# Kernel tuning notes

Measured on AMD Instinct MI355X. Metric: run time of the kernel, lower is better.

The kernel has to match this reference:

```python
import jax, jax.numpy as jnp
import numpy as np

H = 1024   # hidden_size
S = 1024   # seq_length
B = 32     # batch_size


def setup_inputs() -> dict:
    key = jax.random.key(0)
    k1, k2, k3, k4, k5, k6 = jax.random.split(key, 6)
    scale = 1.0 / np.sqrt(3 * H)
    return {
        "encoder_states": jax.random.normal(k1, (S, B, 2 * H), dtype=jnp.float32),
        "hidden": jax.random.normal(k2, (B, H), dtype=jnp.float32),
        "cell": jax.random.normal(k3, (B, H), dtype=jnp.float32),
        "W_attn": jax.random.normal(k4, (H, 3 * H), dtype=jnp.float32) * scale,
        "b_attn": jax.random.normal(k5, (H,), dtype=jnp.float32) * scale,
        "v_w": jax.random.normal(k6, (H,), dtype=jnp.float32) * (1.0 / np.sqrt(H)),
    }


def reference(encoder_states, hidden, cell, W_attn, b_attn, v_w):
    # cell is accepted by the original forward but unused.
    # Split the concat-linear into two projections (mathematically identical,
    # avoids materializing the repeated hidden + concat tensor):
    # cat((hidden_rep, enc), -1) @ W.T == hidden @ W[:, :H].T + enc @ W[:, H:].T
    W_h = W_attn[:, :H]          # [H, H]   multiplies decoder hidden
    W_e = W_attn[:, H:]          # [H, 2H]  multiplies encoder states
    enc = jnp.transpose(encoder_states, (1, 0, 2))          # [B, S, 2H]
    h_proj = hidden @ W_h.T + b_attn                         # [B, H], broadcast over S
    e_proj = jnp.einsum("bse,he->bsh", enc, W_e)             # [B, S, H]
    energy = jnp.tanh(h_proj[:, None, :] + e_proj)           # [B, S, H]
    attention = jnp.einsum("bsh,h->bs", energy, v_w)         # [B, S]
    return jax.nn.softmax(attention, axis=1)
```

## Files before the change

### kernel.cpp

```cpp
#include <hip/hip_runtime.h>
#include <hip/hip_bf16.h>

#define H 1024
#define S 1024
#define B 32
#define K2 2048

typedef unsigned short u16;
typedef __attribute__((ext_vector_type(8))) short short8;
typedef __attribute__((ext_vector_type(8))) unsigned short u16x8;
typedef __attribute__((ext_vector_type(4))) float floatx4;

__device__ __forceinline__ u16 f2bf(float f) {
  unsigned u = __float_as_uint(f);
  u += 0x7FFFu + ((u >> 16) & 1u);
  return (u16)(u >> 16);
}

__device__ __forceinline__ void gld_lds16(const void* g, void* l) {
  __builtin_amdgcn_global_load_lds(
      (const __attribute__((address_space(1))) unsigned int*)g,
      (__attribute__((address_space(3))) unsigned int*)l, 16, 0, 0);
}

__device__ __forceinline__ float tanh_fast(float x) {
  float t = __expf(2.0f * x);
  return 1.0f - 2.0f / (t + 1.0f);
}

__global__ void conv_we_k(const float* __restrict__ W, u16* __restrict__ dst) {
  const int h = blockIdx.x;
  const int t = threadIdx.x * 8;
  const float* sp = W + (size_t)h * 3072 + H + t;
  u16* dp = dst + (size_t)h * K2 + t;
  floatx4 x = *(const floatx4*)sp;
  floatx4 y = *(const floatx4*)(sp + 4);
  u16x8 o;
  o[0] = f2bf(x[0]); o[1] = f2bf(x[1]); o[2] = f2bf(x[2]); o[3] = f2bf(x[3]);
  o[4] = f2bf(y[0]); o[5] = f2bf(y[1]); o[6] = f2bf(y[2]); o[7] = f2bf(y[3]);
  *(u16x8*)dp = o;
}

__global__ void conv_enc_k(const float* __restrict__ enc, u16* __restrict__ dst) {
  const int sb = blockIdx.x;
  const int s = sb >> 5;
  const int b = sb & 31;
  const int t = threadIdx.x * 8;
  const float* sp = enc + (size_t)sb * K2 + t;
  u16* dp = dst + ((size_t)b * S + s) * K2 + t;
  floatx4 x = *(const floatx4*)sp;
  floatx4 y = *(const floatx4*)(sp + 4);
  u16x8 o;
  o[0] = f2bf(x[0]); o[1] = f2bf(x[1]); o[2] = f2bf(x[2]); o[3] = f2bf(x[3]);
  o[4] = f2bf(y[0]); o[5] = f2bf(y[1]); o[6] = f2bf(y[2]); o[7] = f2bf(y[3]);
  *(u16x8*)dp = o;
}

__global__ void hproj_k(const float* __restrict__ hidden, const float* __restrict__ W,
                        const float* __restrict__ b_attn, float* __restrict__ hp) {
  const int lane = threadIdx.x & 63;
  const int h = (blockIdx.x * blockDim.x + threadIdx.x) >> 6;
  float wr[16];
#pragma unroll
  for (int i = 0; i < 16; i++) wr[i] = W[(size_t)h * 3072 + lane + i * 64];
  for (int b = 0; b < B; b++) {
    float d = 0.f;
#pragma unroll
    for (int i = 0; i < 16; i++) d = fmaf(wr[i], hidden[b * H + lane + i * 64], d);
#pragma unroll
    for (int off = 32; off; off >>= 1) d += __shfl_xor(d, off);
    if (lane == 0) hp[b * H + h] = d + b_attn[h];
  }
}

#define BM 128
#define BN 128
#define BK 64

__global__ __launch_bounds__(256) void gemm_bf16_k(
    const u16* __restrict__ A,
    const u16* __restrict__ Bw,
    const float* __restrict__ hp, const float* __restrict__ vw,
    float* __restrict__ attn) {
  __shared__ __align__(16) u16 sA[BM * BK];
  __shared__ __align__(16) u16 sB[BN * BK];
  const int tid = threadIdx.x;
  const int bid = blockIdx.x;
  const int ntile = bid >> 8;
  const int b = (bid & 255) >> 3;
  const int mtile = bid & 7;
  const int s0 = mtile * BM;
  const int h0 = ntile * BN;

  const int lane = tid & 63;
  const int wv = tid >> 6;
  const int wm = (wv >> 1) * 64;
  const int wn = (wv & 1) * 64;
  const int fr = lane & 15;
  const int kgrp = lane >> 4;

  const int lr8 = lane >> 3;
  const int sg8 = lane & 7;
  const int ssw = (sg8 ^ lr8) << 3;

  const u16* Abase = A + (size_t)b * S * K2;

  floatx4 acc[4][4];
#pragma unroll
  for (int i = 0; i < 4; i++)
#pragma unroll
    for (int j = 0; j < 4; j++) acc[i][j] = (floatx4){0.f, 0.f, 0.f, 0.f};

  for (int k0 = 0; k0 < K2; k0 += BK) {
    __syncthreads();
#pragma unroll
    for (int p = 0; p < 4; p++) {
      const int r = p * 32 + wv * 8 + lr8;
      gld_lds16(Abase + (size_t)(s0 + r) * K2 + k0 + ssw,
                (char*)sA + (p * 32 + wv * 8) * 128);
      gld_lds16(Bw + (size_t)(h0 + r) * K2 + k0 + ssw,
                (char*)sB + (p * 32 + wv * 8) * 128);
    }
    __syncthreads();

#pragma unroll
    for (int kh = 0; kh < 2; ++kh) {
      const int ks = kh * 4 + kgrp;
      short8 af[4], bfr[4];
#pragma unroll
      for (int mf = 0; mf < 4; mf++) {
        const int R = wm + mf * 16 + fr;
        af[mf] = *(const short8*)&sA[R * BK + ((ks ^ (R & 7)) << 3)];
      }
#pragma unroll
      for (int nf = 0; nf < 4; nf++) {
        const int R = wn + nf * 16 + fr;
        bfr[nf] = *(const short8*)&sB[R * BK + ((ks ^ (R & 7)) << 3)];
      }
#pragma unroll
      for (int mf = 0; mf < 4; mf++)
#pragma unroll
        for (int nf = 0; nf < 4; nf++)
          acc[mf][nf] =
              __builtin_amdgcn_mfma_f32_16x16x32_bf16(af[mf], bfr[nf], acc[mf][nf], 0, 0, 0);
    }
  }

  const int col = fr;
  const int rgrp = lane >> 4;
  float hv[4], vv[4];
#pragma unroll
  for (int nf = 0; nf < 4; nf++) {
    const int h = h0 + wn + nf * 16 + col;
    hv[nf] = hp[b * H + h];
    vv[nf] = vw[h];
  }
#pragma unroll
  for (int mf = 0; mf < 4; mf++) {
#pragma unroll
    for (int r = 0; r < 4; r++) {
      float part = 0.f;
#pragma unroll
      for (int nf = 0; nf < 4; nf++) part += tanh_fast(acc[mf][nf][r] + hv[nf]) * vv[nf];
      part += __shfl_xor(part, 1);
      part += __shfl_xor(part, 2);
      part += __shfl_xor(part, 4);
      part += __shfl_xor(part, 8);
      if (col == 0)
        atomicAdd(&attn[b * S + s0 + wm + mf * 16 + rgrp * 4 + r], part);
    }
  }
}

__global__ void softmax_k(const float* __restrict__ attn, float* __restrict__ out) {
  __shared__ float red[8];
  const int b = blockIdx.x;
  const int tid = threadIdx.x;
  const float* row = attn + b * S;
  float v[4];
#pragma unroll
  for (int i = 0; i < 4; i++) v[i] = row[tid + i * 256];
  float m = fmaxf(fmaxf(v[0], v[1]), fmaxf(v[2], v[3]));
#pragma unroll
  for (int off = 32; off; off >>= 1) m = fmaxf(m, __shfl_xor(m, off));
  if ((tid & 63) == 0) red[tid >> 6] = m;
  __syncthreads();
  m = fmaxf(fmaxf(red[0], red[1]), fmaxf(red[2], red[3]));
  float e[4], sum = 0.f;
#pragma unroll
  for (int i = 0; i < 4; i++) { e[i] = __expf(v[i] - m); sum += e[i]; }
#pragma unroll
  for (int off = 32; off; off >>= 1) sum += __shfl_xor(sum, off);
  __syncthreads();
  if ((tid & 63) == 0) red[4 + (tid >> 6)] = sum;
  __syncthreads();
  sum = red[4] + red[5] + red[6] + red[7];
  const float inv = 1.0f / sum;
#pragma unroll
  for (int i = 0; i < 4; i++) out[b * S + tid + i * 256] = e[i] * inv;
}

extern "C" void kernel_launch(void* const* d_in, const int* in_sizes, int n_in,
                              void* d_out, int out_size, void* d_ws, size_t ws_size,
                              hipStream_t stream) {
  const float* enc    = (const float*)d_in[0];
  const float* hidden = (const float*)d_in[1];
  const float* W_attn = (const float*)d_in[3];
  const float* b_attn = (const float*)d_in[4];
  const float* v_w    = (const float*)d_in[5];
  float* out = (float*)d_out;

  char* ws = (char*)d_ws;
  float* attn = (float*)ws;
  float* hp   = (float*)(ws + 131072);
  u16* Web    = (u16*)(ws + 262144);
  u16* encb   = (u16*)(ws + 4456448);

  hipMemsetAsync(attn, 0, B * S * sizeof(float), stream);
  conv_we_k<<<H, 256, 0, stream>>>(W_attn, Web);
  hproj_k<<<256, 256, 0, stream>>>(hidden, W_attn, b_attn, hp);
  conv_enc_k<<<S * B, 256, 0, stream>>>(enc, encb);
  gemm_bf16_k<<<2048, 256, 0, stream>>>(encb, Web, hp, v_w, attn);
  softmax_k<<<B, 256, 0, stream>>>(attn, out);
}
```

Measured before the change: 638.2 us.

## Replace GEMM with 256x256-tile 8-phase double-buffered pipelined MFMA kernel

Swaps the 128x128 single-buffered GEMM for a 256x256 tile kernel with 8 waves and double-buffered LDS, split into quarter-tiles. Global-to-LDS loads for later k-steps are interleaved with MFMA phases, using explicit barriers, vmcnt waits and setprio. This is meant to hide load latency and raise arithmetic intensity per tile. In exchange it uses far more registers (8x4 accumulators per wave) and more LDS, leaves only 512 blocks, and relies on hand-tuned wait counts that must be correct.

Result: faster. 573.8 us (-10.1%).

```diff
diff --git a/kernel.cpp b/kernel.cpp
--- a/kernel.cpp
+++ b/kernel.cpp
@@ -73,101 +73,141 @@
   }
 }
 
-#define BM 128
-#define BN 128
+#define BM 256
+#define BN 256
 #define BK 64
-
-__global__ __launch_bounds__(256) void gemm_bf16_k(
+#define NKT 32
+
+#define STG_A(BUF, MH, KT)                                                    \
+  { _Pragma("unroll") for (int c_ = 0; c_ < 2; ++c_) {                        \
+      const int ri_ = c_ * 64 + srow;                                         \
+      const int rg_ = ((ri_ >> 6) << 7) + (MH) * 64 + (ri_ & 63);             \
+      const int lg_ = sseg ^ (ri_ & 7);                                       \
+      gld_lds16(Ab + (size_t)(s0 + rg_) * K2 + (KT) * BK + (lg_ << 3),        \
+                (char*)&sA[BUF][MH][0] + c_ * 8192 + wv * 1024); } }
+
+#define STG_B(BUF, NH, KT)                                                    \
+  { _Pragma("unroll") for (int c_ = 0; c_ < 2; ++c_) {                        \
+      const int ri_ = c_ * 64 + srow;                                         \
+      const int rg_ = ((ri_ >> 5) << 6) + (NH) * 32 + (ri_ & 31);             \
+      const int lg_ = sseg ^ (ri_ & 7);                                       \
+      gld_lds16(Bw + (size_t)(h0 + rg_) * K2 + (KT) * BK + (lg_ << 3),        \
+                (char*)&sB[BUF][NH][0] + c_ * 8192 + wv * 1024); } }
+
+#define PHASE(BUF, MH, NH, STAGE, DRAIN)                                      \
+  {                                                                           \
+    short8 af_[4][2], bf_[2][2];                                              \
+    _Pragma("unroll") for (int m_ = 0; m_ < 4; ++m_)                          \
+      _Pragma("unroll") for (int k_ = 0; k_ < 2; ++k_)                        \
+        af_[m_][k_] = *(const short8*)(&sA[BUF][MH][0] + aoff[m_][k_]);       \
+    _Pragma("unroll") for (int n_ = 0; n_ < 2; ++n_)                          \
+      _Pragma("unroll") for (int k_ = 0; k_ < 2; ++k_)                        \
+        bf_[n_][k_] = *(const short8*)(&sB[BUF][NH][0] + boff[n_][k_]);       \
+    STAGE                                                                     \
+    __builtin_amdgcn_s_barrier();                                             \
+    asm volatile("s_waitcnt lgkmcnt(0)" ::: "memory");                        \
+    __builtin_amdgcn_sched_barrier(0);                                        \
+    __builtin_amdgcn_s_setprio(1);                                            \
+    _Pragma("unroll") for (int k_ = 0; k_ < 2; ++k_)                          \
+      _Pragma("unroll") for (int m_ = 0; m_ < 4; ++m_)                        \
+        _Pragma("unroll") for (int n_ = 0; n_ < 2; ++n_)                      \
+          acc[(MH) * 4 + m_][(NH) * 2 + n_] =                                 \
+              __builtin_amdgcn_mfma_f32_16x16x32_bf16(                        \
+                  af_[m_][k_], bf_[n_][k_],                                   \
+                  acc[(MH) * 4 + m_][(NH) * 2 + n_], 0, 0, 0);                \
+    __builtin_amdgcn_s_setprio(0);                                            \
+    DRAIN                                                                     \
+    __builtin_amdgcn_s_barrier();                                             \
+  }
+
+__global__ __launch_bounds__(512, 2) void gemm_8ph_k(
     const u16* __restrict__ A,
     const u16* __restrict__ Bw,
     const float* __restrict__ hp, const float* __restrict__ vw,
     float* __restrict__ attn) {
-  __shared__ __align__(16) u16 sA[BM * BK];
-  __shared__ __align__(16) u16 sB[BN * BK];
+  __shared__ __align__(16) u16 sA[2][2][128 * 64];
+  __shared__ __align__(16) u16 sB[2][2][128 * 64];
+
   const int tid = threadIdx.x;
+  const int lane = tid & 63;
+  const int wv = tid >> 6;
+  const int wr = wv >> 2;
+  const int wc = wv & 3;
+  const int fr = lane & 15;
+  const int kgrp = lane >> 4;
+  const int srow = wv * 8 + (lane >> 3);
+  const int sseg = lane & 7;
+
   const int bid = blockIdx.x;
-  const int ntile = bid >> 8;
-  const int b = (bid & 255) >> 3;
-  const int mtile = bid & 7;
+  const int ntile = bid >> 7;
+  const int b = (bid >> 2) & 31;
+  const int mtile = bid & 3;
   const int s0 = mtile * BM;
   const int h0 = ntile * BN;
 
-  const int lane = tid & 63;
-  const int wv = tid >> 6;
-  const int wm = (wv >> 1) * 64;
-  const int wn = (wv & 1) * 64;
-  const int fr = lane & 15;
-  const int kgrp = lane >> 4;
-
-  const int lr8 = lane >> 3;
-  const int sg8 = lane & 7;
-  const int ssw = (sg8 ^ lr8) << 3;
-
-  const u16* Abase = A + (size_t)b * S * K2;
-
-  floatx4 acc[4][4];
-#pragma unroll
-  for (int i = 0; i < 4; i++)
-#pragma unroll
-    for (int j = 0; j < 4; j++) acc[i][j] = (floatx4){0.f, 0.f, 0.f, 0.f};
-
-  for (int k0 = 0; k0 < K2; k0 += BK) {
-    __syncthreads();
-#pragma unroll
-    for (int p = 0; p < 4; p++) {
-      const int r = p * 32 + wv * 8 + lr8;
-      gld_lds16(Abase + (size_t)(s0 + r) * K2 + k0 + ssw,
-                (char*)sA + (p * 32 + wv * 8) * 128);
-      gld_lds16(Bw + (size_t)(h0 + r) * K2 + k0 + ssw,
-                (char*)sB + (p * 32 + wv * 8) * 128);
-    }
-    __syncthreads();
-
-#pragma unroll
-    for (int kh = 0; kh < 2; ++kh) {
-      const int ks = kh * 4 + kgrp;
-      short8 af[4], bfr[4];
-#pragma unroll
-      for (int mf = 0; mf < 4; mf++) {
-        const int R = wm + mf * 16 + fr;
-        af[mf] = *(const short8*)&sA[R * BK + ((ks ^ (R & 7)) << 3)];
-      }
-#pragma unroll
-      for (int nf = 0; nf < 4; nf++) {
-        const int R = wn + nf * 16 + fr;
-        bfr[nf] = *(const short8*)&sB[R * BK + ((ks ^ (R & 7)) << 3)];
-      }
-#pragma unroll
-      for (int mf = 0; mf < 4; mf++)
-#pragma unroll
-        for (int nf = 0; nf < 4; nf++)
-          acc[mf][nf] =
-              __builtin_amdgcn_mfma_f32_16x16x32_bf16(af[mf], bfr[nf], acc[mf][nf], 0, 0, 0);
-    }
+  const u16* Ab = A + (size_t)b * S * K2;
+
+  int aoff[4][2], boff[2][2];
+#pragma unroll
+  for (int m = 0; m < 4; ++m)
+#pragma unroll
+    for (int k = 0; k < 2; ++k)
+      aoff[m][k] = (wr * 64 + m * 16 + fr) * 64 + ((((k << 2) + kgrp) ^ (fr & 7)) << 3);
+#pragma unroll
+  for (int n = 0; n < 2; ++n)
+#pragma unroll
+    for (int k = 0; k < 2; ++k)
+      boff[n][k] = (wc * 32 + n * 16 + fr) * 64 + ((((k << 2) + kgrp) ^ (fr & 7)) << 3);
+
+  floatx4 acc[8][4];
+#pragma unroll
+  for (int i = 0; i < 8; ++i)
+#pragma unroll
+    for (int j = 0; j < 4; ++j) acc[i][j] = (floatx4){0.f, 0.f, 0.f, 0.f};
+
+  STG_B(0, 0, 0) STG_A(0, 0, 0) STG_A(0, 1, 0) STG_B(0, 1, 0)
+  STG_B(1, 0, 1) STG_A(1, 0, 1)
+  asm volatile("s_waitcnt vmcnt(4)" ::: "memory");
+  __builtin_amdgcn_s_barrier();
+
+  for (int it = 0; it < 16; ++it) {
+    const int t1 = 2 * it + 1, t2 = 2 * it + 2, t3 = 2 * it + 3;
+    const bool Lst = (it == 15);
+    PHASE(0, 0, 0, STG_A(1, 1, t1), )
+    PHASE(0, 1, 0, STG_B(1, 1, t1), )
+    PHASE(0, 0, 1, if (!Lst) { STG_B(0, 0, t2) }, )
+    PHASE(0, 1, 1, if (!Lst) { STG_A(0, 0, t2) },
+          if (Lst) { asm volatile("s_waitcnt vmcnt(0)" ::: "memory"); }
+          else     { asm volatile("s_waitcnt vmcnt(4)" ::: "memory"); } )
+    PHASE(1, 0, 0, if (!Lst) { STG_A(0, 1, t2) }, )
+    PHASE(1, 1, 0, if (!Lst) { STG_B(0, 1, t2) }, )
+    PHASE(1, 0, 1, if (!Lst) { STG_B(1, 0, t3) }, )
+    PHASE(1, 1, 1, if (!Lst) { STG_A(1, 0, t3) },
+          if (!Lst) { asm volatile("s_waitcnt vmcnt(4)" ::: "memory"); } )
   }
 
   const int col = fr;
   const int rgrp = lane >> 4;
   float hv[4], vv[4];
 #pragma unroll
-  for (int nf = 0; nf < 4; nf++) {
-    const int h = h0 + wn + nf * 16 + col;
+  for (int nf = 0; nf < 4; ++nf) {
+    const int h = h0 + wc * 64 + nf * 16 + col;
     hv[nf] = hp[b * H + h];
     vv[nf] = vw[h];
   }
 #pragma unroll
-  for (int mf = 0; mf < 4; mf++) {
-#pragma unroll
-    for (int r = 0; r < 4; r++) {
+  for (int mf = 0; mf < 8; ++mf) {
+#pragma unroll
+    for (int r = 0; r < 4; ++r) {
       float part = 0.f;
 #pragma unroll
-      for (int nf = 0; nf < 4; nf++) part += tanh_fast(acc[mf][nf][r] + hv[nf]) * vv[nf];
+      for (int nf = 0; nf < 4; ++nf) part += tanh_fast(acc[mf][nf][r] + hv[nf]) * vv[nf];
       part += __shfl_xor(part, 1);
       part += __shfl_xor(part, 2);
       part += __shfl_xor(part, 4);
       part += __shfl_xor(part, 8);
       if (col == 0)
-        atomicAdd(&attn[b * S + s0 + wm + mf * 16 + rgrp * 4 + r], part);
+        atomicAdd(&attn[b * S + s0 + wr * 128 + mf * 16 + rgrp * 4 + r], part);
     }
   }
 }
@@ -220,6 +260,6 @@
   conv_we_k<<<H, 256, 0, stream>>>(W_attn, Web);
   hproj_k<<<256, 256, 0, stream>>>(hidden, W_attn, b_attn, hp);
   conv_enc_k<<<S * B, 256, 0, stream>>>(enc, encb);
-  gemm_bf16_k<<<2048, 256, 0, stream>>>(encb, Web, hp, v_w, attn);
+  gemm_8ph_k<<<512, 512, 0, stream>>>(encb, Web, hp, v_w, attn);
   softmax_k<<<B, 256, 0, stream>>>(attn, out);
 }
```
